# Kernel optimization log

Measured on AMD Instinct MI355X. Metric: run time of the kernel, lower is better.

## Reference

```python
import jax, jax.numpy as jnp
from jax import lax
import numpy as np

B, A, D = 4, 512, 729   # batch, num_angles, detector pixels
H, W = 512, 512         # reconstruction volume


def setup_inputs() -> dict:
    key = jax.random.key(0)
    sino = jax.random.normal(key, (B, A, D), dtype=jnp.float32)
    vol_spacing = np.array([1.0, 1.0], dtype=np.float32)          # (sy, sx)
    det_spacing = np.array([1.0], dtype=np.float32)
    vol_origin = np.array([-(H - 1) / 2.0, -(W - 1) / 2.0], dtype=np.float32)
    det_origin = np.array([-(D - 1) / 2.0], dtype=np.float32)
    angles = jnp.linspace(0.0, jnp.pi, A, endpoint=False, dtype=jnp.float32)
    return {
        "input": sino,
        "volume_shape": np.array([H, W], dtype=np.int64),
        "volume_origin": jnp.asarray(vol_origin),
        "detector_origin": jnp.asarray(det_origin),
        "volume_spacing": jnpp if False else jnp.asarray(vol_spacing),
        "detector_spacing": jnp.asarray(det_spacing),
        "trajectory": angles,
    }


def _backproject(sino, vol_shape, vol_origin, det_origin, vol_spacing, det_spacing, angles):
    h, w = int(vol_shape[0]), int(vol_shape[1])
    d = sino.shape[-1]
    ys = vol_origin[0] + jnp.arange(h, dtype=sino.dtype) * vol_spacing[0]  # [H]
    xs = vol_origin[1] + jnp.arange(w, dtype=sino.dtype) * vol_spacing[1]  # [W]

    def step(acc, per_angle):
        theta, sino_a = per_angle                      # scalar, [B, D]
        # ray coordinate s = x*cos(theta) + y*sin(theta) for every voxel
        s = xs[None, :] * jnp.cos(theta) + ys[:, None] * jnp.sin(theta)  # [H, W]
        u = (s - det_origin[0]) / det_spacing[0]       # continuous detector index
        u0 = jnp.floor(u)
        frac = u - u0
        i0 = u0.astype(jnp.int32)
        i1 = i0 + 1
        valid0 = (i0 >= 0) & (i0 < d)
        valid1 = (i1 >= 0) & (i1 < d)
        i0c = jnp.clip(i0, 0, d - 1)
        i1c = jnp.clip(i1, 0, d - 1)
        v0 = sino_a[:, i0c]                            # [B, H, W] gather
        v1 = sino_a[:, i1c]                            # [B, H, W] gather
        contrib = (jnp.where(valid0, (1.0 - frac) * v0, 0.0)
                   + jnp.where(valid1, frac * v1, 0.0))
        return acc + contrib, None

    acc0 = jnp.zeros((sino.shape[0], h, w), dtype=sino.dtype)
    out, _ = lax.scan(step, acc0, (angles, jnp.swapaxes(sino, 0, 1)))
    return out


def reference(input, volume_shape, volume_origin, detector_origin,
              volume_spacing, detector_spacing, trajectory):
    return _backproject(input, volume_shape, volume_origin, detector_origin,
                        volume_spacing, detector_spacing, trajectory)
```

## Files before the change

kernel.cpp:

```cpp
#include <hip/hip_runtime.h>
#include <hip/hip_fp16.h>

#define BB 4
#define AA 512
#define ZS 8
#define AH (AA / ZS)
#define DD 729
#define HH 512
#define WW 512
#define CH 4
#define NC (AH / CH)
#define WIN 64
#define AD (AA * DD)
#define GX (WW / 64)
#define GY (HH / 32)

typedef float        f4v  __attribute__((ext_vector_type(4)));
typedef unsigned int u4v8 __attribute__((ext_vector_type(4), aligned(8)));
typedef unsigned int u2v8 __attribute__((ext_vector_type(2), aligned(8)));

__device__ inline float buf_load1(__amdgpu_buffer_rsrc_t r, int elem) {
    union { unsigned int u; float f; } c;
    c.u = __builtin_amdgcn_raw_buffer_load_b32(r, elem * 4, 0, 0);
    return c.f;
}
__device__ inline __half2 h2bc(unsigned int x) {
    return __builtin_bit_cast(__half2, x);
}
__device__ inline unsigned int pk2u(float a, float b) {
    return __builtin_bit_cast(unsigned int, __builtin_amdgcn_cvt_pkrtz(a, b));
}

__global__ __launch_bounds__(256, 4) void bp_kernel(
    const float* __restrict__ sino,
    const float* __restrict__ vol_origin,
    const float* __restrict__ det_origin,
    const float* __restrict__ vol_spacing,
    const float* __restrict__ det_spacing,
    const float* __restrict__ angles,
    float* __restrict__ out)
{
    __shared__ f4v          s_csk[4][AH];
    __shared__ int          s_s0[4][AH];
    __shared__ __align__(16) unsigned int s_win[4][CH * WIN * 2];

    const int tid  = threadIdx.y * 16 + threadIdx.x;
    const int lane = tid & 63;
    const int wv   = tid >> 6;

    const int nlin = (int)blockIdx.x + GX * ((int)blockIdx.y + GY * (int)blockIdx.z);
    const int zsl  = nlin & (ZS - 1);
    const int mm   = nlin >> 3;
    const int bxx  = mm & (GX - 1);
    const int byy  = mm >> 3;

    const float inv_ds = 1.0f / det_spacing[0];
    const int abase = zsl * AH;

    const int x0 = bxx * 64 + wv * 16;
    const int y0 = byy * 32;
    const float vsx = vol_spacing[1], vsy = vol_spacing[0];
    const float off = -det_origin[0] * inv_ds;
    const float xc = vol_origin[1] + ((float)x0 + 7.5f) * vsx;
    const float yc = vol_origin[0] + ((float)y0 + 15.5f) * vsy;

    {
        const int a = lane;
        float th = angles[abase + a];
        float c = cosf(th) * inv_ds;
        float s = sinf(th) * inv_ds;
        float uc = fmaf(xc, c, fmaf(yc, s, off));
        int s0 = min(max((int)uc - (WIN / 2), 0), DD - WIN);
        f4v k;
        k.x = c; k.y = s; k.z = off - (float)s0; k.w = 4.0f * vsy * s;
        s_csk[wv][a] = k;
        s_s0[wv][a]  = s0;
    }
    __threadfence_block();

    const int ix  = x0 + threadIdx.x;
    const int iy0 = y0 + (threadIdx.y & 3);
    const float xw = vol_origin[1] + (float)ix * vsx;
    const float yw = vol_origin[0] + (float)iy0 * vsy;

    const __amdgpu_buffer_rsrc_t rsrc = __builtin_amdgcn_make_buffer_rsrc(
        (void*)sino, (short)0, BB * AA * DD * 4, 0x00020000);

    f4v acc0 = {0.f,0.f,0.f,0.f}, acc1 = {0.f,0.f,0.f,0.f};
    f4v acc2 = {0.f,0.f,0.f,0.f}, acc3 = {0.f,0.f,0.f,0.f};
    f4v acc4 = {0.f,0.f,0.f,0.f}, acc5 = {0.f,0.f,0.f,0.f};
    f4v acc6 = {0.f,0.f,0.f,0.f}, acc7 = {0.f,0.f,0.f,0.f};

    const __half2 hz   = h2bc(0u);
    const __half2 one2 = h2bc(0x3C003C00u);
    __half2 h01_0 = hz, h23_0 = hz, h01_1 = hz, h23_1 = hz;
    __half2 h01_2 = hz, h23_2 = hz, h01_3 = hz, h23_3 = hz;
    __half2 h01_4 = hz, h23_4 = hz, h01_5 = hz, h23_5 = hz;
    __half2 h01_6 = hz, h23_6 = hz, h01_7 = hz, h23_7 = hz;

    float vA0, vA1, vA2, vA3, vB0, vB1, vB2, vB3;
    float vC0, vC1, vC2, vC3, vD0, vD1, vD2, vD3;

    #define STAGE_LOAD(C)                                                  \
        do {                                                               \
            const int aa = (C) * CH;                                       \
            const int r0 = (abase + aa + 0) * DD + s_s0[wv][aa + 0] + lane;\
            const int r1 = (abase + aa + 1) * DD + s_s0[wv][aa + 1] + lane;\
            const int r2 = (abase + aa + 2) * DD + s_s0[wv][aa + 2] + lane;\
            const int r3 = (abase + aa + 3) * DD + s_s0[wv][aa + 3] + lane;\
            vA0 = buf_load1(rsrc, r0);          vA1 = buf_load1(rsrc, r0 + AD);     \
            vA2 = buf_load1(rsrc, r0 + 2 * AD); vA3 = buf_load1(rsrc, r0 + 3 * AD); \
            vB0 = buf_load1(rsrc, r1);          vB1 = buf_load1(rsrc, r1 + AD);     \
            vB2 = buf_load1(rsrc, r1 + 2 * AD); vB3 = buf_load1(rsrc, r1 + 3 * AD); \
            vC0 = buf_load1(rsrc, r2);          vC1 = buf_load1(rsrc, r2 + AD);     \
            vC2 = buf_load1(rsrc, r2 + 2 * AD); vC3 = buf_load1(rsrc, r2 + 3 * AD); \
            vD0 = buf_load1(rsrc, r3);          vD1 = buf_load1(rsrc, r3 + AD);     \
            vD2 = buf_load1(rsrc, r3 + 2 * AD); vD3 = buf_load1(rsrc, r3 + 3 * AD); \
        } while (0)

    #define CONVERT_WRITE()                                                \
        do {                                                               \
            u2v8 q;                                                        \
            q.x = pk2u(vA0, vA1); q.y = pk2u(vA2, vA3);                    \
            *(u2v8*)&s_win[wv][0 * 128 + 2 * lane] = q;                    \
            q.x = pk2u(vB0, vB1); q.y = pk2u(vB2, vB3);                    \
            *(u2v8*)&s_win[wv][1 * 128 + 2 * lane] = q;                    \
            q.x = pk2u(vC0, vC1); q.y = pk2u(vC2, vC3);                    \
            *(u2v8*)&s_win[wv][2 * 128 + 2 * lane] = q;                    \
            q.x = pk2u(vD0, vD1); q.y = pk2u(vD2, vD3);                    \
            *(u2v8*)&s_win[wv][3 * 128 + 2 * lane] = q;                    \
        } while (0)

    #define LERP(U, H01, H23)                                              \
        do {                                                               \
            const int   li = (int)(U);                                     \
            const float fr = __builtin_amdgcn_fractf(U);                   \
            const __half2 fr2 = h2bc(pk2u(fr, fr));                        \
            const __half2 om2 = __hsub2(one2, fr2);                        \
            const u4v8 t = *(const u4v8*)&s_win[wv][(j * WIN + li) * 2];   \
            H01 = __hfma2(h2bc(t.x), om2, __hfma2(h2bc(t.z), fr2, H01));   \
            H23 = __hfma2(h2bc(t.y), om2, __hfma2(h2bc(t.w), fr2, H23));   \
        } while (0)

    #define WIDEN(H01, H23, ACC)                                           \
        do {                                                               \
            (ACC).x += __low2float(H01);  (ACC).y += __high2float(H01);    \
            (ACC).z += __low2float(H23);  (ACC).w += __high2float(H23);    \
            H01 = hz; H23 = hz;                                            \
        } while (0)

    STAGE_LOAD(0);
    for (int c = 0; c < NC; ++c) {
        __threadfence_block();
        CONVERT_WRITE();
        __threadfence_block();
        if (c + 1 < NC) STAGE_LOAD(c + 1);
        #pragma unroll
        for (int j = 0; j < CH; ++j) {
            const f4v k = s_csk[wv][c * CH + j];
            float u = fmaf(xw, k.x, fmaf(yw, k.y, k.z));
            LERP(u, h01_0, h23_0); u += k.w;
            LERP(u, h01_1, h23_1); u += k.w;
            LERP(u, h01_2, h23_2); u += k.w;
            LERP(u, h01_3, h23_3); u += k.w;
            LERP(u, h01_4, h23_4); u += k.w;
            LERP(u, h01_5, h23_5); u += k.w;
            LERP(u, h01_6, h23_6); u += k.w;
            LERP(u, h01_7, h23_7);
        }
        WIDEN(h01_0, h23_0, acc0);
        WIDEN(h01_1, h23_1, acc1);
        WIDEN(h01_2, h23_2, acc2);
        WIDEN(h01_3, h23_3, acc3);
        WIDEN(h01_4, h23_4, acc4);
        WIDEN(h01_5, h23_5, acc5);
        WIDEN(h01_6, h23_6, acc6);
        WIDEN(h01_7, h23_7, acc7);
    }
    #undef STAGE_LOAD
    #undef CONVERT_WRITE
    #undef LERP
    #undef WIDEN

    const size_t HW = (size_t)HH * WW;
    #define OUT4(ACC, ROWOFF)                                              \
        do {                                                               \
            const size_t o = (size_t)(iy0 + (ROWOFF)) * WW + ix;           \
            unsafeAtomicAdd(&out[o],          (ACC).x);                    \
            unsafeAtomicAdd(&out[o + HW],     (ACC).y);                    \
            unsafeAtomicAdd(&out[o + 2 * HW], (ACC).z);                    \
            unsafeAtomicAdd(&out[o + 3 * HW], (ACC).w);                    \
        } while (0)
    OUT4(acc0, 0);
    OUT4(acc1, 4);
    OUT4(acc2, 8);
    OUT4(acc3, 12);
    OUT4(acc4, 16);
    OUT4(acc5, 20);
    OUT4(acc6, 24);
    OUT4(acc7, 28);
    #undef OUT4
}

extern "C" void kernel_launch(void* const* d_in, const int* in_sizes, int n_in,
                              void* d_out, int out_size, void* d_ws, size_t ws_size,
                              hipStream_t stream) {
    const float* sino        = (const float*)d_in[0];
    const float* vol_origin  = (const float*)d_in[2];
    const float* det_origin  = (const float*)d_in[3];
    const float* vol_spacing = (const float*)d_in[4];
    const float* det_spacing = (const float*)d_in[5];
    const float* angles      = (const float*)d_in[6];
    float* out = (float*)d_out;

    hipMemsetAsync(d_out, 0, (size_t)out_size * sizeof(float), stream);

    dim3 block(16, 16, 1);
    dim3 grid(GX, GY, ZS);
    bp_kernel<<<grid, block, 0, stream>>>(sino, vol_origin, det_origin,
                                          vol_spacing, det_spacing, angles, out);
}
```

Measured before the change: 127.4 us.

## Split each block's angle range across wave pairs and merge partial sums in LDS

Each block now covers a 32-wide x tile, with two waves per 16-column tile. Each wave in a pair handles half of the block's 64 angles, and the halves are combined through shared memory before the atomic adds. This doubles the block count and shortens each wave's serial angle loop, aiming for more parallelism and half as many global atomics per wave pair. The costs are extra barriers, LDS traffic, duplicated setup per block, and a launch bound raised to 8 blocks per CU, which may squeeze registers.

```diff
diff --git a/kernel.cpp b/kernel.cpp
--- a/kernel.cpp
+++ b/kernel.cpp
@@ -4,15 +4,15 @@
 #define BB 4
 #define AA 512
 #define ZS 8
-#define AH (AA / ZS)
+#define AHW 32
 #define DD 729
 #define HH 512
 #define WW 512
 #define CH 4
-#define NC (AH / CH)
+#define NC (AHW / CH)
 #define WIN 64
 #define AD (AA * DD)
-#define GX (WW / 64)
+#define GX (WW / 32)
 #define GY (HH / 32)
 
 typedef float        f4v  __attribute__((ext_vector_type(4)));
@@ -31,7 +31,7 @@
     return __builtin_bit_cast(unsigned int, __builtin_amdgcn_cvt_pkrtz(a, b));
 }
 
-__global__ __launch_bounds__(256, 4) void bp_kernel(
+__global__ __launch_bounds__(256, 8) void bp_kernel(
     const float* __restrict__ sino,
     const float* __restrict__ vol_origin,
     const float* __restrict__ det_origin,
@@ -40,31 +40,34 @@
     const float* __restrict__ angles,
     float* __restrict__ out)
 {
-    __shared__ f4v          s_csk[4][AH];
-    __shared__ int          s_s0[4][AH];
+    __shared__ f4v          s_csk[4][AHW];
+    __shared__ int          s_s0[4][AHW];
     __shared__ __align__(16) unsigned int s_win[4][CH * WIN * 2];
-
-    const int tid  = threadIdx.y * 16 + threadIdx.x;
-    const int lane = tid & 63;
-    const int wv   = tid >> 6;
+    __shared__ f4v          s_mrg[2][64][4];
+
+    const int tid   = threadIdx.y * 16 + threadIdx.x;
+    const int lane  = tid & 63;
+    const int wv    = tid >> 6;
+    const int tile  = wv >> 1;
+    const int ahalf = wv & 1;
 
     const int nlin = (int)blockIdx.x + GX * ((int)blockIdx.y + GY * (int)blockIdx.z);
     const int zsl  = nlin & (ZS - 1);
     const int mm   = nlin >> 3;
     const int bxx  = mm & (GX - 1);
-    const int byy  = mm >> 3;
+    const int byy  = mm >> 4;
 
     const float inv_ds = 1.0f / det_spacing[0];
-    const int abase = zsl * AH;
-
-    const int x0 = bxx * 64 + wv * 16;
+    const int abase = zsl * 64 + ahalf * AHW;
+
+    const int x0 = bxx * 32 + tile * 16;
     const int y0 = byy * 32;
     const float vsx = vol_spacing[1], vsy = vol_spacing[0];
     const float off = -det_origin[0] * inv_ds;
     const float xc = vol_origin[1] + ((float)x0 + 7.5f) * vsx;
     const float yc = vol_origin[0] + ((float)y0 + 15.5f) * vsy;
 
-    {
+    if (lane < AHW) {
         const int a = lane;
         float th = angles[abase + a];
         float c = cosf(th) * inv_ds;
@@ -182,24 +185,45 @@
     #undef LERP
     #undef WIDEN
 
-    const size_t HW = (size_t)HH * WW;
-    #define OUT4(ACC, ROWOFF)                                              \
-        do {                                                               \
-            const size_t o = (size_t)(iy0 + (ROWOFF)) * WW + ix;           \
-            unsafeAtomicAdd(&out[o],          (ACC).x);                    \
-            unsafeAtomicAdd(&out[o + HW],     (ACC).y);                    \
-            unsafeAtomicAdd(&out[o + 2 * HW], (ACC).z);                    \
-            unsafeAtomicAdd(&out[o + 3 * HW], (ACC).w);                    \
-        } while (0)
-    OUT4(acc0, 0);
-    OUT4(acc1, 4);
-    OUT4(acc2, 8);
-    OUT4(acc3, 12);
-    OUT4(acc4, 16);
-    OUT4(acc5, 20);
-    OUT4(acc6, 24);
-    OUT4(acc7, 28);
-    #undef OUT4
+    if (ahalf) {
+        s_mrg[tile][lane][0] = acc0;  s_mrg[tile][lane][1] = acc1;
+        s_mrg[tile][lane][2] = acc2;  s_mrg[tile][lane][3] = acc3;
+    }
+    __syncthreads();
+    if (!ahalf) {
+        acc0 += s_mrg[tile][lane][0]; acc1 += s_mrg[tile][lane][1];
+        acc2 += s_mrg[tile][lane][2]; acc3 += s_mrg[tile][lane][3];
+    }
+    __syncthreads();
+    if (ahalf) {
+        s_mrg[tile][lane][0] = acc4;  s_mrg[tile][lane][1] = acc5;
+        s_mrg[tile][lane][2] = acc6;  s_mrg[tile][lane][3] = acc7;
+    }
+    __syncthreads();
+
+    if (!ahalf) {
+        acc4 += s_mrg[tile][lane][0]; acc5 += s_mrg[tile][lane][1];
+        acc6 += s_mrg[tile][lane][2]; acc7 += s_mrg[tile][lane][3];
+
+        const size_t HW = (size_t)HH * WW;
+        #define OUT4(ACC, ROWOFF)                                          \
+            do {                                                           \
+                const size_t o = (size_t)(iy0 + (ROWOFF)) * WW + ix;       \
+                unsafeAtomicAdd(&out[o],          (ACC).x);                \
+                unsafeAtomicAdd(&out[o + HW],     (ACC).y);                \
+                unsafeAtomicAdd(&out[o + 2 * HW], (ACC).z);                \
+                unsafeAtomicAdd(&out[o + 3 * HW], (ACC).w);                \
+            } while (0)
+        OUT4(acc0, 0);
+        OUT4(acc1, 4);
+        OUT4(acc2, 8);
+        OUT4(acc3, 12);
+        OUT4(acc4, 16);
+        OUT4(acc5, 20);
+        OUT4(acc6, 24);
+        OUT4(acc7, 28);
+        #undef OUT4
+    }
 }
 
 extern "C" void kernel_launch(void* const* d_in, const int* in_sizes, int n_in,
```

Result: slower. 272.7 us (+114.0%).
